# Kernel tuning notes

Measured on AMD Instinct MI355X. Metric: run time of the kernel, lower is better.

Reference implementation:

```python
import jax, jax.numpy as jnp
import numpy as np

BETA = 10.0
EPS = 1e-6


def setup_inputs() -> dict:
    key = jax.random.key(0)
    k0, k1 = jax.random.split(key)
    f0 = jax.random.normal(k0, (4, 256, 64, 64), dtype=jnp.float32)
    f1 = jax.random.normal(k1, (4, 256, 64, 64), dtype=jnp.float32)
    return {"f0": f0, "f1": f1}


def _l2norm(x, axis):
    norm = jnp.sqrt(jnp.sum(x * x, axis=axis, keepdims=True))
    return x / jnp.maximum(norm, EPS)


def reference(f0, f1):
    B, C, Ha, Wa = f0.shape
    _, _, Hb, Wb = f1.shape
    # [B, HaWa, C] and [B, HbWb, C]
    a = f0.reshape(B, C, Ha * Wa).transpose(0, 2, 1)
    b = f1.reshape(B, C, Hb * Wb).transpose(0, 2, 1)
    a = _l2norm(a, axis=2)
    b = _l2norm(b, axis=2)
    # cosine similarity scaled by beta: [B, HaWa, HbWb]
    sim = jnp.einsum('bnc,bmc->bnm', a, b) * BETA
    attn = jax.nn.softmax(sim, axis=2)
    # target coords (x, y) of image1 grid: [HbWb, 2]
    ys = jnp.arange(Hb, dtype=f0.dtype)
    xs = jnp.arange(Wb, dtype=f0.dtype)
    yy, xx = jnp.meshgrid(ys, xs, indexing='ij')
    coords = jnp.stack([xx.reshape(-1), yy.reshape(-1)], axis=1)
    tgt = jnp.einsum('bnm,mk->bnk', attn, coords)
    warp_c = tgt.reshape(B, Ha, Wa, 2)
    cert_c = jnp.max(attn, axis=2).reshape(B, Ha, Wa)
    return (warp_c, cert_c)
```

## Files before the change

### kernel.cpp

```cpp
#include <hip/hip_runtime.h>
#include <hip/hip_bf16.h>

#define BETA_LOG2E 14.426950408889634f
#define EPSN 1e-6f

typedef __bf16 bf16x8 __attribute__((ext_vector_type(8)));
typedef float  f32x4  __attribute__((ext_vector_type(4)));

static __device__ inline unsigned short f2bf(float f) {
    __hip_bfloat16 h = __float2bfloat16(f);
    return __builtin_bit_cast(unsigned short, h);
}
static __device__ inline float bf2f(unsigned short u) {
    unsigned int b = ((unsigned int)u) << 16;
    return __builtin_bit_cast(float, b);
}

__global__ __launch_bounds__(256) void k_norm_transpose(
    const float* __restrict__ f0, const float* __restrict__ f1,
    unsigned short* __restrict__ aT, unsigned short* __restrict__ bT)
{
    __shared__ unsigned short tile[256][65];
    __shared__ float partial[4][64];
    __shared__ float inv_l[64];

    int idx   = blockIdx.x;
    int which = idx >> 8;
    int rem   = idx & 255;
    int b     = rem >> 6;
    int n0    = (rem & 63) * 64;
    const float* src = which ? f1 : f0;
    unsigned short* dst = which ? bT : aT;

    int t   = threadIdx.x;
    int n_l = t & 63;
    int cg  = t >> 6;

    float ss = 0.f;
#pragma unroll 4
    for (int i = 0; i < 64; ++i) {
        int c = i * 4 + cg;
        float v = src[(b * 256 + c) * 4096 + n0 + n_l];
        ss += v * v;
        tile[c][n_l] = f2bf(v);
    }
    partial[cg][n_l] = ss;
    __syncthreads();
    if (t < 64) {
        float s = partial[0][t] + partial[1][t] + partial[2][t] + partial[3][t];
        inv_l[t] = 1.0f / fmaxf(sqrtf(s), EPSN);
    }
    __syncthreads();

#pragma unroll 4
    for (int j = 0; j < 16; ++j) {
        int nw = (t & 3) + (j & 3) * 4 + (t >> 6) * 16;
        int u  = ((t >> 2) & 15) + (j >> 2) * 16;
        int c  = u * 4;
        float inv = inv_l[nw];
        unsigned short o0 = f2bf(bf2f(tile[c + 0][nw]) * inv);
        unsigned short o1 = f2bf(bf2f(tile[c + 1][nw]) * inv);
        unsigned short o2 = f2bf(bf2f(tile[c + 2][nw]) * inv);
        unsigned short o3 = f2bf(bf2f(tile[c + 3][nw]) * inv);
        uint2 val;
        val.x = (unsigned int)o0 | ((unsigned int)o1 << 16);
        val.y = (unsigned int)o2 | ((unsigned int)o3 << 16);
        *reinterpret_cast<uint2*>(&dst[((size_t)(b * 4096 + n0 + nw)) * 256 + c]) = val;
    }
}

__global__ __launch_bounds__(256) void k_flash(
    const unsigned short* __restrict__ aT, const unsigned short* __restrict__ bT,
    float* __restrict__ stats)
{
    __shared__ unsigned short kbuf[64 * 272];

    int idx   = blockIdx.x;
    int xcd   = idx & 7;
    int batch = xcd >> 1;
    int sub   = ((idx >> 3) << 1) | (xcd & 1);
    int qt    = sub >> 2;
    int ks    = sub & 3;

    int t    = threadIdx.x;
    int w    = t >> 6;
    int lane = t & 63;
    int quad = lane >> 4;
    int l15  = lane & 15;
    int q0w  = qt * 128 + w * 32;
    int k0   = ks * 1024;

    bf16x8 afrag[2][8];
#pragma unroll
    for (int s = 0; s < 2; ++s) {
        const unsigned short* ap =
            aT + ((size_t)(batch * 4096 + q0w + s * 16 + l15)) * 256 + quad * 8;
#pragma unroll
        for (int kk = 0; kk < 8; ++kk)
            afrag[s][kk] = *reinterpret_cast<const bf16x8*>(ap + kk * 32);
    }

    float Z[8], Sx[8], Sy[8], Pm[8];
#pragma unroll
    for (int i = 0; i < 8; ++i) { Z[i] = 0.f; Sx[i] = 0.f; Sy[i] = 0.f; Pm[i] = 0.f; }

    for (int ch = 0; ch < 16; ++ch) {
        int kbase = k0 + ch * 64;
        const unsigned short* gsrc = bT + ((size_t)(batch * 4096 + kbase)) * 256;
#pragma unroll
        for (int i = 0; i < 8; ++i) {
            int h = i * 2048 + t * 8;
            uint4 v = *reinterpret_cast<const uint4*>(gsrc + h);
            int key  = i * 8 + (t >> 5);
            int gran = t & 31;
            *reinterpret_cast<uint4*>(&kbuf[key * 272 + gran * 8]) = v;
        }
        __syncthreads();

#pragma unroll
        for (int nt = 0; nt < 4; ++nt) {
            f32x4 acc0 = {0.f, 0.f, 0.f, 0.f};
            f32x4 acc1 = {0.f, 0.f, 0.f, 0.f};
            const unsigned short* lp = &kbuf[(nt * 16 + l15) * 272 + quad * 8];
#pragma unroll
            for (int kk = 0; kk < 8; ++kk) {
                bf16x8 bfrag = *reinterpret_cast<const bf16x8*>(lp + kk * 32);
                acc0 = __builtin_amdgcn_mfma_f32_16x16x32_bf16(afrag[0][kk], bfrag, acc0, 0, 0, 0);
                acc1 = __builtin_amdgcn_mfma_f32_16x16x32_bf16(afrag[1][kk], bfrag, acc1, 0, 0, 0);
            }
            int key  = kbase + nt * 16 + l15;
            float kx = (float)(key & 63);
            float ky = (float)(key >> 6);
#pragma unroll
            for (int r = 0; r < 4; ++r) {
                float p0 = exp2f(acc0[r] * BETA_LOG2E);
                Z[r]  += p0;  Sx[r] += p0 * kx;  Sy[r] += p0 * ky;
                Pm[r] = fmaxf(Pm[r], p0);
                float p1 = exp2f(acc1[r] * BETA_LOG2E);
                Z[4 + r]  += p1;  Sx[4 + r] += p1 * kx;  Sy[4 + r] += p1 * ky;
                Pm[4 + r] = fmaxf(Pm[4 + r], p1);
            }
        }
        __syncthreads();
    }

#pragma unroll
    for (int i = 0; i < 8; ++i) {
#pragma unroll
        for (int m = 1; m <= 8; m <<= 1) {
            Z[i]  += __shfl_xor(Z[i], m);
            Sx[i] += __shfl_xor(Sx[i], m);
            Sy[i] += __shfl_xor(Sy[i], m);
            Pm[i]  = fmaxf(Pm[i], __shfl_xor(Pm[i], m));
        }
    }
    if (l15 == 0) {
#pragma unroll
        for (int s = 0; s < 2; ++s)
#pragma unroll
            for (int r = 0; r < 4; ++r) {
                int q = q0w + s * 16 + quad * 4 + r;
                f32x4 st = {Z[s * 4 + r], Sx[s * 4 + r], Sy[s * 4 + r], Pm[s * 4 + r]};
                *reinterpret_cast<f32x4*>(&stats[((size_t)(batch * 4096 + q) * 4 + ks) * 4]) = st;
            }
    }
}

__global__ __launch_bounds__(256) void k_finalize(
    const float* __restrict__ stats, float* __restrict__ out)
{
    int q = blockIdx.x * 256 + threadIdx.x;
    const f32x4* s = reinterpret_cast<const f32x4*>(stats + (size_t)q * 16);
    f32x4 a0 = s[0], a1 = s[1], a2 = s[2], a3 = s[3];
    float Z  = a0.x + a1.x + a2.x + a3.x;
    float Sx = a0.y + a1.y + a2.y + a3.y;
    float Sy = a0.z + a1.z + a2.z + a3.z;
    float Pm = fmaxf(fmaxf(a0.w, a1.w), fmaxf(a2.w, a3.w));
    float invZ = 1.0f / Z;
    out[q * 2 + 0]  = Sx * invZ;
    out[q * 2 + 1]  = Sy * invZ;
    out[32768 + q]  = Pm * invZ;
}

extern "C" void kernel_launch(void* const* d_in, const int* in_sizes, int n_in,
                              void* d_out, int out_size, void* d_ws, size_t ws_size,
                              hipStream_t stream)
{
    const float* f0 = (const float*)d_in[0];
    const float* f1 = (const float*)d_in[1];
    unsigned short* aT = (unsigned short*)d_ws;
    unsigned short* bT = aT + (size_t)4 * 4096 * 256;
    float* stats = (float*)(bT + (size_t)4 * 4096 * 256);
    float* out = (float*)d_out;

    hipLaunchKernelGGL(k_norm_transpose, dim3(512), dim3(256), 0, stream, f0, f1, aT, bT);
    hipLaunchKernelGGL(k_flash,          dim3(512), dim3(256), 0, stream, aT, bT, stats);
    hipLaunchKernelGGL(k_finalize,       dim3(64),  dim3(256), 0, stream, stats, out);
}
```

Measured before the change: 131.1 us.

## Vectorize norm-transpose, split keys eightfold, and trim per-element softmax epilogue work

The normalize/transpose kernel now reads float4 vectors, packs bf16 pairs and writes them into an XOR-swizzled shared tile with 16-byte stores, replacing the padded scalar tile. The flash kernel splits the key dimension into 8 chunks instead of 4, giving 1024 blocks with launch bounds requesting 4 blocks per CU. Its epilogue tracks the max of raw scores rather than exp values and accumulates the y-coordinate once per 64-key chunk through a per-chunk partial Z. The finalize kernel reduces 8 partials per query instead of 4, which doubles the stats traffic.

```diff
diff --git a/kernel.cpp b/kernel.cpp
--- a/kernel.cpp
+++ b/kernel.cpp
@@ -20,8 +20,8 @@
     const float* __restrict__ f0, const float* __restrict__ f1,
     unsigned short* __restrict__ aT, unsigned short* __restrict__ bT)
 {
-    __shared__ unsigned short tile[256][65];
-    __shared__ float partial[4][64];
+    __shared__ unsigned short tile[64 * 256];
+    __shared__ float partial[16][64];
     __shared__ float inv_l[64];
 
     int idx   = blockIdx.x;
@@ -32,44 +32,67 @@
     const float* src = which ? f1 : f0;
     unsigned short* dst = which ? bT : aT;
 
-    int t   = threadIdx.x;
-    int n_l = t & 63;
-    int cg  = t >> 6;
-
-    float ss = 0.f;
-#pragma unroll 4
-    for (int i = 0; i < 64; ++i) {
-        int c = i * 4 + cg;
-        float v = src[(b * 256 + c) * 4096 + n0 + n_l];
-        ss += v * v;
-        tile[c][n_l] = f2bf(v);
-    }
-    partial[cg][n_l] = ss;
+    int t  = threadIdx.x;
+    int nq = t & 15;
+    int cg = t >> 4;
+
+    const float* sp = src + ((size_t)(b * 256 + cg * 16)) * 4096 + n0 + nq * 4;
+
+    f32x4 ss = {0.f, 0.f, 0.f, 0.f};
+#pragma unroll
+    for (int ch2 = 0; ch2 < 2; ++ch2) {
+        unsigned int pk[4][4];
+#pragma unroll
+        for (int i = 0; i < 8; ++i) {
+            f32x4 v = *reinterpret_cast<const f32x4*>(sp + (ch2 * 8 + i) * 4096);
+            ss += v * v;
+#pragma unroll
+            for (int j = 0; j < 4; ++j) {
+                unsigned int h = f2bf(v[j]);
+                if (i & 1) pk[j][i >> 1] |= h << 16;
+                else       pk[j][i >> 1]  = h;
+            }
+        }
+        int cb = cg * 2 + ch2;
+#pragma unroll
+        for (int j = 0; j < 4; ++j) {
+            int n = nq * 4 + j;
+            int s = cb ^ nq;
+            *reinterpret_cast<uint4*>(&tile[n * 256 + s * 8]) =
+                *reinterpret_cast<const uint4*>(pk[j]);
+        }
+    }
+    *reinterpret_cast<f32x4*>(&partial[cg][nq * 4]) = ss;
     __syncthreads();
     if (t < 64) {
-        float s = partial[0][t] + partial[1][t] + partial[2][t] + partial[3][t];
+        float s = 0.f;
+#pragma unroll
+        for (int k = 0; k < 16; ++k) s += partial[k][t];
         inv_l[t] = 1.0f / fmaxf(sqrtf(s), EPSN);
     }
     __syncthreads();
 
-#pragma unroll 4
-    for (int j = 0; j < 16; ++j) {
-        int nw = (t & 3) + (j & 3) * 4 + (t >> 6) * 16;
-        int u  = ((t >> 2) & 15) + (j >> 2) * 16;
-        int c  = u * 4;
-        float inv = inv_l[nw];
-        unsigned short o0 = f2bf(bf2f(tile[c + 0][nw]) * inv);
-        unsigned short o1 = f2bf(bf2f(tile[c + 1][nw]) * inv);
-        unsigned short o2 = f2bf(bf2f(tile[c + 2][nw]) * inv);
-        unsigned short o3 = f2bf(bf2f(tile[c + 3][nw]) * inv);
-        uint2 val;
-        val.x = (unsigned int)o0 | ((unsigned int)o1 << 16);
-        val.y = (unsigned int)o2 | ((unsigned int)o3 << 16);
-        *reinterpret_cast<uint2*>(&dst[((size_t)(b * 4096 + n0 + nw)) * 256 + c]) = val;
-    }
-}
-
-__global__ __launch_bounds__(256) void k_flash(
+#pragma unroll
+    for (int it = 0; it < 8; ++it) {
+        int n  = it * 8 + (t >> 5);
+        int cb = t & 31;
+        int s  = cb ^ (n >> 2);
+        uint4 v = *reinterpret_cast<const uint4*>(&tile[n * 256 + s * 8]);
+        float inv = inv_l[n];
+        unsigned int o[4];
+#pragma unroll
+        for (int k = 0; k < 4; ++k) {
+            unsigned int u = (&v.x)[k];
+            unsigned short lo = f2bf(bf2f((unsigned short)(u & 0xffffu)) * inv);
+            unsigned short hi = f2bf(bf2f((unsigned short)(u >> 16)) * inv);
+            o[k] = (unsigned int)lo | ((unsigned int)hi << 16);
+        }
+        *reinterpret_cast<uint4*>(&dst[((size_t)(b * 4096 + n0 + n)) * 256 + cb * 8]) =
+            *reinterpret_cast<const uint4*>(o);
+    }
+}
+
+__global__ __launch_bounds__(256, 4) void k_flash(
     const unsigned short* __restrict__ aT, const unsigned short* __restrict__ bT,
     float* __restrict__ stats)
 {
@@ -79,8 +102,8 @@
     int xcd   = idx & 7;
     int batch = xcd >> 1;
     int sub   = ((idx >> 3) << 1) | (xcd & 1);
-    int qt    = sub >> 2;
-    int ks    = sub & 3;
+    int qt    = sub >> 3;
+    int ks    = sub & 7;
 
     int t    = threadIdx.x;
     int w    = t >> 6;
@@ -88,7 +111,7 @@
     int quad = lane >> 4;
     int l15  = lane & 15;
     int q0w  = qt * 128 + w * 32;
-    int k0   = ks * 1024;
+    int k0   = ks * 512;
 
     bf16x8 afrag[2][8];
 #pragma unroll
@@ -100,11 +123,11 @@
             afrag[s][kk] = *reinterpret_cast<const bf16x8*>(ap + kk * 32);
     }
 
-    float Z[8], Sx[8], Sy[8], Pm[8];
-#pragma unroll
-    for (int i = 0; i < 8; ++i) { Z[i] = 0.f; Sx[i] = 0.f; Sy[i] = 0.f; Pm[i] = 0.f; }
-
-    for (int ch = 0; ch < 16; ++ch) {
+    float Z[8], Sx[8], Sy[8], Sm[8];
+#pragma unroll
+    for (int i = 0; i < 8; ++i) { Z[i] = 0.f; Sx[i] = 0.f; Sy[i] = 0.f; Sm[i] = -1e30f; }
+
+    for (int ch = 0; ch < 8; ++ch) {
         int kbase = k0 + ch * 64;
         const unsigned short* gsrc = bT + ((size_t)(batch * 4096 + kbase)) * 256;
 #pragma unroll
@@ -117,6 +140,10 @@
         }
         __syncthreads();
 
+        float Zc[8];
+#pragma unroll
+        for (int i = 0; i < 8; ++i) Zc[i] = 0.f;
+
 #pragma unroll
         for (int nt = 0; nt < 4; ++nt) {
             f32x4 acc0 = {0.f, 0.f, 0.f, 0.f};
@@ -128,18 +155,22 @@
                 acc0 = __builtin_amdgcn_mfma_f32_16x16x32_bf16(afrag[0][kk], bfrag, acc0, 0, 0, 0);
                 acc1 = __builtin_amdgcn_mfma_f32_16x16x32_bf16(afrag[1][kk], bfrag, acc1, 0, 0, 0);
             }
-            int key  = kbase + nt * 16 + l15;
-            float kx = (float)(key & 63);
-            float ky = (float)(key >> 6);
+            float kx = (float)(nt * 16 + l15);
 #pragma unroll
             for (int r = 0; r < 4; ++r) {
                 float p0 = exp2f(acc0[r] * BETA_LOG2E);
-                Z[r]  += p0;  Sx[r] += p0 * kx;  Sy[r] += p0 * ky;
-                Pm[r] = fmaxf(Pm[r], p0);
+                Zc[r]     += p0;  Sx[r]     += p0 * kx;
+                Sm[r]      = fmaxf(Sm[r], acc0[r]);
                 float p1 = exp2f(acc1[r] * BETA_LOG2E);
-                Z[4 + r]  += p1;  Sx[4 + r] += p1 * kx;  Sy[4 + r] += p1 * ky;
-                Pm[4 + r] = fmaxf(Pm[4 + r], p1);
-            }
+                Zc[4 + r] += p1;  Sx[4 + r] += p1 * kx;
+                Sm[4 + r]  = fmaxf(Sm[4 + r], acc1[r]);
+            }
+        }
+        float ky = (float)(kbase >> 6);
+#pragma unroll
+        for (int i = 0; i < 8; ++i) {
+            Z[i]  += Zc[i];
+            Sy[i]  = fmaf(ky, Zc[i], Sy[i]);
         }
         __syncthreads();
     }
@@ -151,7 +182,7 @@
             Z[i]  += __shfl_xor(Z[i], m);
             Sx[i] += __shfl_xor(Sx[i], m);
             Sy[i] += __shfl_xor(Sy[i], m);
-            Pm[i]  = fmaxf(Pm[i], __shfl_xor(Pm[i], m));
+            Sm[i]  = fmaxf(Sm[i], __shfl_xor(Sm[i], m));
         }
     }
     if (l15 == 0) {
@@ -160,8 +191,9 @@
 #pragma unroll
             for (int r = 0; r < 4; ++r) {
                 int q = q0w + s * 16 + quad * 4 + r;
-                f32x4 st = {Z[s * 4 + r], Sx[s * 4 + r], Sy[s * 4 + r], Pm[s * 4 + r]};
-                *reinterpret_cast<f32x4*>(&stats[((size_t)(batch * 4096 + q) * 4 + ks) * 4]) = st;
+                f32x4 st = {Z[s * 4 + r], Sx[s * 4 + r], Sy[s * 4 + r],
+                            exp2f(Sm[s * 4 + r] * BETA_LOG2E)};
+                *reinterpret_cast<f32x4*>(&stats[((size_t)(batch * 4096 + q) * 8 + ks) * 4]) = st;
             }
     }
 }
@@ -170,12 +202,13 @@
     const float* __restrict__ stats, float* __restrict__ out)
 {
     int q = blockIdx.x * 256 + threadIdx.x;
-    const f32x4* s = reinterpret_cast<const f32x4*>(stats + (size_t)q * 16);
-    f32x4 a0 = s[0], a1 = s[1], a2 = s[2], a3 = s[3];
-    float Z  = a0.x + a1.x + a2.x + a3.x;
-    float Sx = a0.y + a1.y + a2.y + a3.y;
-    float Sy = a0.z + a1.z + a2.z + a3.z;
-    float Pm = fmaxf(fmaxf(a0.w, a1.w), fmaxf(a2.w, a3.w));
+    const f32x4* s = reinterpret_cast<const f32x4*>(stats + (size_t)q * 32);
+    float Z = 0.f, Sx = 0.f, Sy = 0.f, Pm = 0.f;
+#pragma unroll
+    for (int k = 0; k < 8; ++k) {
+        f32x4 a = s[k];
+        Z += a.x; Sx += a.y; Sy += a.z; Pm = fmaxf(Pm, a.w);
+    }
     float invZ = 1.0f / Z;
     out[q * 2 + 0]  = Sx * invZ;
     out[q * 2 + 1]  = Sy * invZ;
@@ -193,7 +226,7 @@
     float* stats = (float*)(bT + (size_t)4 * 4096 * 256);
     float* out = (float*)d_out;
 
-    hipLaunchKernelGGL(k_norm_transpose, dim3(512), dim3(256), 0, stream, f0, f1, aT, bT);
-    hipLaunchKernelGGL(k_flash,          dim3(512), dim3(256), 0, stream, aT, bT, stats);
-    hipLaunchKernelGGL(k_finalize,       dim3(64),  dim3(256), 0, stream, stats, out);
-}
+    hipLaunchKernelGGL(k_norm_transpose, dim3(512),  dim3(256), 0, stream, f0, f1, aT, bT);
+    hipLaunchKernelGGL(k_flash,          dim3(1024), dim3(256), 0, stream, aT, bT, stats);
+    hipLaunchKernelGGL(k_finalize,       dim3(64),   dim3(256), 0, stream, stats, out);
+}
```

New measurement: 165.9 us. 26.5% more time.
